# Optimization experiments

Measured on AMD Instinct MI355X. Metric: run time of the kernel, lower is better.

The kernel has to match this reference:

```python
import jax, jax.numpy as jnp
import numpy as np

NEG_SLOPE = 0.01  # nn.LeakyReLU default negative_slope


def setup_inputs() -> dict:
    key = jax.random.key(0)
    k1, k2 = jax.random.split(key)
    B, N, D = 32, 128, 128
    embeddings = jax.random.normal(k1, (B, N, D), dtype=jnp.float32)
    # nn.Linear(em_dim, 1): weight [1, D] -> stored as [D], bias [1]
    att_w = jax.random.normal(k2, (D,), dtype=jnp.float32) * (1.0 / np.sqrt(D))
    att_b = jnp.zeros((1,), dtype=jnp.float32)
    return {"embeddings": embeddings, "att_w": att_w, "att_b": att_b}


def reference(embeddings, att_w, att_b):
    # query[b,i,j,d] = e[b,i,d]; key[b,i,j,d] = e[b,j,d]
    # value = query * key : [B, N, N, D]
    value = embeddings[:, :, None, :] * embeddings[:, None, :, :]
    # Linear(D -> 1): scores[b,i,j] = sum_d value[b,i,j,d] * w[d] + b
    scores = jnp.einsum('bijd,d->bij', value, att_w) + att_b[0]
    scores = jnp.where(scores >= 0, scores, NEG_SLOPE * scores)  # LeakyReLU
    # dropout is identity in eval mode
    alphas = jax.nn.softmax(scores, axis=-1)[..., None]  # [B, N, N, 1]
    return alphas, value
```

## Files before the change

### kernel.cpp

```cpp
#include <hip/hip_runtime.h>
#include <cstddef>

#define B_ 32
#define N_ 128
#define D_ 128
#define NEG_SLOPE 0.01f

__global__ void __launch_bounds__(256)
fused_value_attn_kernel(const float* __restrict__ e,
                        const float* __restrict__ w,
                        const float* __restrict__ bias,
                        float* __restrict__ alphas,
                        float* __restrict__ value) {
    const int bi = blockIdx.x;
    const int b  = bi >> 7;
    const int t  = threadIdx.x;
    const int d4 = t & 31;
    const int jg = t >> 5;

    __shared__ float sc[N_];
    __shared__ float red[N_];

    const float4 w4  = *reinterpret_cast<const float4*>(w + (d4 << 2));
    const float4 ei4 = *reinterpret_cast<const float4*>(
        e + (size_t)bi * D_ + (d4 << 2));
    const float bias0 = bias[0];

    float4* __restrict__ vout = reinterpret_cast<float4*>(
        value + (size_t)bi * N_ * D_);

#pragma unroll 4
    for (int jj = 0; jj < 16; ++jj) {
        const int j = (jj << 3) + jg;
        const float4 ej4 = *reinterpret_cast<const float4*>(
            e + ((size_t)((b << 7) | j)) * D_ + (d4 << 2));

        float4 v4;
        v4.x = ei4.x * ej4.x;
        v4.y = ei4.y * ej4.y;
        v4.z = ei4.z * ej4.z;
        v4.w = ei4.w * ej4.w;

        vout[(j << 5) + d4] = v4;

        float p = v4.x * w4.x + v4.y * w4.y + v4.z * w4.z + v4.w * w4.w;
        p += __shfl_xor(p, 1);
        p += __shfl_xor(p, 2);
        p += __shfl_xor(p, 4);
        p += __shfl_xor(p, 8);
        p += __shfl_xor(p, 16);
        if (d4 == 0) sc[j] = p;
    }
    __syncthreads();

    float s = 0.f, ex = 0.f;
    if (t < N_) {
        s = sc[t] + bias0;
        s = (s >= 0.f) ? s : NEG_SLOPE * s;
        red[t] = s;
    }
    __syncthreads();
#pragma unroll
    for (int off = 64; off > 0; off >>= 1) {
        if (t < off) red[t] = fmaxf(red[t], red[t + off]);
        __syncthreads();
    }
    const float m = red[0];
    __syncthreads();
    if (t < N_) { ex = expf(s - m); red[t] = ex; }
    __syncthreads();
#pragma unroll
    for (int off = 64; off > 0; off >>= 1) {
        if (t < off) red[t] += red[t + off];
        __syncthreads();
    }
    if (t < N_) alphas[(size_t)bi * N_ + t] = ex / red[0];
}

extern "C" void kernel_launch(void* const* d_in, const int* in_sizes, int n_in,
                              void* d_out, int out_size, void* d_ws, size_t ws_size,
                              hipStream_t stream) {
    const float* e    = (const float*)d_in[0];
    const float* w    = (const float*)d_in[1];
    const float* bias = (const float*)d_in[2];

    float* out    = (float*)d_out;
    float* alphas = out;
    float* value  = out + (size_t)B_ * N_ * N_;

    fused_value_attn_kernel<<<B_ * N_, 256, 0, stream>>>(e, w, bias, alphas, value);
}
```

Baseline: 49.72 us.

## Decouple score dot products from value stores and use nontemporal writes

Splits the kernel into a pure value-store loop that uses nontemporal stores, followed by a separate score computation. Scores are computed as dot(e_j, e_i*w), with e_i*w precomputed in shared memory. Each thread sums half of one row's dot product instead of doing a cross-lane shuffle reduction per j. The loop is also fully unrolled. The second pass rereads e rows from memory, which should mostly hit cache, and the per-thread strided row reads may coalesce poorly.

```diff
diff --git a/kernel.cpp b/kernel.cpp
--- a/kernel.cpp
+++ b/kernel.cpp
@@ -5,6 +5,8 @@
 #define N_ 128
 #define D_ 128
 #define NEG_SLOPE 0.01f
+
+typedef float v4f __attribute__((ext_vector_type(4)));
 
 __global__ void __launch_bounds__(256)
 fused_value_attn_kernel(const float* __restrict__ e,
@@ -18,44 +20,45 @@
     const int d4 = t & 31;
     const int jg = t >> 5;
 
-    __shared__ float sc[N_];
+    __shared__ float h[D_];
+    __shared__ float ph[256];
     __shared__ float red[N_];
 
-    const float4 w4  = *reinterpret_cast<const float4*>(w + (d4 << 2));
-    const float4 ei4 = *reinterpret_cast<const float4*>(
-        e + (size_t)bi * D_ + (d4 << 2));
-    const float bias0 = bias[0];
+    const v4f* __restrict__ e4 = reinterpret_cast<const v4f*>(e);
+    const v4f ei4 = e4[(size_t)bi * 32 + d4];
 
-    float4* __restrict__ vout = reinterpret_cast<float4*>(
+    v4f* __restrict__ vout = reinterpret_cast<v4f*>(
         value + (size_t)bi * N_ * D_);
 
-#pragma unroll 4
+#pragma unroll
     for (int jj = 0; jj < 16; ++jj) {
         const int j = (jj << 3) + jg;
-        const float4 ej4 = *reinterpret_cast<const float4*>(
-            e + ((size_t)((b << 7) | j)) * D_ + (d4 << 2));
+        const v4f ej4 = e4[((size_t)((b << 7) | j)) * 32 + d4];
+        const v4f v4 = ei4 * ej4;
+        __builtin_nontemporal_store(v4, &vout[(j << 5) + d4]);
+    }
 
-        float4 v4;
-        v4.x = ei4.x * ej4.x;
-        v4.y = ei4.y * ej4.y;
-        v4.z = ei4.z * ej4.z;
-        v4.w = ei4.w * ej4.w;
+    if (t < N_) h[t] = e[(size_t)bi * D_ + t] * w[t];
+    __syncthreads();
 
-        vout[(j << 5) + d4] = v4;
-
-        float p = v4.x * w4.x + v4.y * w4.y + v4.z * w4.z + v4.w * w4.w;
-        p += __shfl_xor(p, 1);
-        p += __shfl_xor(p, 2);
-        p += __shfl_xor(p, 4);
-        p += __shfl_xor(p, 8);
-        p += __shfl_xor(p, 16);
-        if (d4 == 0) sc[j] = p;
+    const int j2   = t & 127;
+    const int half = t >> 7;
+    const float* __restrict__ ejrow = e + ((size_t)((b << 7) | j2)) * D_ + (half << 6);
+    const float* __restrict__ hrow  = h + (half << 6);
+    float p = 0.f;
+#pragma unroll
+    for (int q = 0; q < 16; ++q) {
+        const v4f ejv = *reinterpret_cast<const v4f*>(ejrow + (q << 2));
+        const v4f hv  = *reinterpret_cast<const v4f*>(hrow + (q << 2));
+        const v4f pr  = hv * ejv;
+        p += pr.x + pr.y + pr.z + pr.w;
     }
+    ph[t] = p;
     __syncthreads();
 
     float s = 0.f, ex = 0.f;
     if (t < N_) {
-        s = sc[t] + bias0;
+        s = ph[t] + ph[t + 128] + bias[0];
         s = (s >= 0.f) ? s : NEG_SLOPE * s;
         red[t] = s;
     }
```

New measurement: 59.14 us. 18.9% more time.
